# Kernel optimization log

Measured on AMD Instinct MI355X. Metric: run time of the kernel, lower is better.

## Reference

```python
import jax, jax.numpy as jnp
import numpy as np

EPS = 1e-6

def _rms(x, w):
    # RMSNorm over last dim with learned scale w
    var = jnp.mean(x * x, axis=-1, keepdims=True)
    return x * jax.lax.rsqrt(var + EPS) * w

def _split_heads(x, h):
    b, l, hd = x.shape
    return x.reshape(b, l, h, hd // h).transpose(0, 2, 1, 3)  # b h l d

def setup_inputs() -> dict:
    key = jax.random.key(0)
    ks = jax.random.split(key, 12)
    D = 2048          # hidden_size == ip_hidden_states_dim
    H = 16            # n_heads
    Dh = 128          # head_dim
    T = 1280          # timesteps_emb_dim
    B, L, Lip = 2, 2048, 512
    s = 0.02
    return {
        "ip_hidden_states": jax.random.normal(ks[0], (B, Lip, D), jnp.float32),
        "img_query": jax.random.normal(ks[1], (B, L, D), jnp.float32),
        "img_key": jax.random.normal(ks[2], (B, L, D), jnp.float32),
        "img_value": jax.random.normal(ks[3], (B, L, D), jnp.float32),
        "t_emb": jax.random.normal(ks[4], (B, T), jnp.float32),
        "W_ada": jax.random.normal(ks[5], (2 * D, T), jnp.float32) * s,
        "b_ada": jax.random.normal(ks[6], (2 * D,), jnp.float32) * s,
        "W_k_ip": jax.random.normal(ks[7], (D, D), jnp.float32) * s,
        "W_v_ip": jax.random.normal(ks[8], (D, D), jnp.float32) * s,
        "w_q": jnp.ones((Dh,), jnp.float32),
        "w_k": jnp.ones((Dh,), jnp.float32),
        "w_ipk": jnp.ones((Dh,), jnp.float32),
        "n_heads": H,
    }

def reference(ip_hidden_states, img_query, img_key, img_value, t_emb,
              W_ada, b_ada, W_k_ip, W_v_ip, w_q, w_k, w_ipk, n_heads):
    D = img_query.shape[-1]
    # AdaLayerNorm (mode='normal'): silu -> linear -> shift/scale, LN(no affine)
    emb = jax.nn.silu(t_emb) @ W_ada.T + b_ada          # [B, 2D]
    shift, scale = emb[:, :D], emb[:, D:]
    x = ip_hidden_states
    mu = jnp.mean(x, axis=-1, keepdims=True)
    var = jnp.mean((x - mu) ** 2, axis=-1, keepdims=True)
    xn = (x - mu) * jax.lax.rsqrt(var + 1e-6)
    ip_n = xn * (1.0 + scale[:, None, :]) + shift[:, None, :]
    # K/V projections for IP tokens
    ip_key = ip_n @ W_k_ip.T
    ip_value = ip_n @ W_v_ip.T
    # split heads
    q = _split_heads(img_query, n_heads)   # b h L d
    k = _split_heads(img_key, n_heads)
    v = _split_heads(img_value, n_heads)
    kip = _split_heads(ip_key, n_heads)    # b h Lip d
    vip = _split_heads(ip_value, n_heads)
    # RMSNorms
    q = _rms(q, w_q)
    k = _rms(k, w_k)
    kip = _rms(kip, w_ipk)
    # concat image + IP along sequence
    kcat = jnp.concatenate([k, kip], axis=2)
    vcat = jnp.concatenate([v, vip], axis=2)
    # SDPA
    d = q.shape[-1]
    scores = jnp.einsum('bhld,bhmd->bhlm', q, kcat) / jnp.sqrt(jnp.asarray(d, q.dtype))
    attn = jax.nn.softmax(scores, axis=-1)
    out = jnp.einsum('bhlm,bhmd->bhld', attn, vcat)
    b, h, l, dh = out.shape
    return out.transpose(0, 2, 1, 3).reshape(b, l, h * dh)
```

## Files before the change

### kernel.cpp

```cpp
#include <hip/hip_runtime.h>
#include <hip/hip_bf16.h>

typedef __attribute__((ext_vector_type(8))) __bf16 bf16x8;
typedef __attribute__((ext_vector_type(2))) __bf16 bf16x2;
typedef __attribute__((ext_vector_type(4))) float floatx4;
typedef __attribute__((ext_vector_type(2))) unsigned int uint2v;

#define DEV static __device__ __forceinline__

typedef __attribute__((address_space(1))) const unsigned int gu32;
typedef __attribute__((address_space(3))) unsigned int lu32;

DEV void dma16(const void* g, void* l) {
  __builtin_amdgcn_global_load_lds((gu32*)g, (lu32*)l, 16, 0, 0);
}

DEV unsigned short f2bf(float f) {
  unsigned int u = __float_as_uint(f);
  u += 0x7fffu + ((u >> 16) & 1u);
  return (unsigned short)(u >> 16);
}

DEV unsigned int pk_bf16(float a, float b) {
#if __has_builtin(__builtin_amdgcn_cvt_pk_bf16_f32)
  bf16x2 r = __builtin_amdgcn_cvt_pk_bf16_f32(a, b);
  union { bf16x2 v; unsigned int u; } c; c.v = r;
  return c.u;
#else
  return (unsigned int)f2bf(a) | ((unsigned int)f2bf(b) << 16);
#endif
}

DEV float wred_sum(float v) {
#pragma unroll
  for (int o = 32; o > 0; o >>= 1) v += __shfl_xor(v, o, 64);
  return v;
}

DEV floatx4 mfma32(bf16x8 a, bf16x8 b, floatx4 c) {
  return __builtin_amdgcn_mfma_f32_16x16x32_bf16(a, b, c, 0, 0, 0);
}

#if __has_builtin(__builtin_amdgcn_permlane32_swap) && __has_builtin(__builtin_amdgcn_permlane16_swap)
#define HAS_PLSWAP 1
DEV void p32sw(unsigned int& a, unsigned int& b) {
  uint2v r = __builtin_amdgcn_permlane32_swap(a, b, false, false);
  a = r[0]; b = r[1];
}
DEV void p16sw(unsigned int& a, unsigned int& b) {
  uint2v r = __builtin_amdgcn_permlane16_swap(a, b, false, false);
  a = r[0]; b = r[1];
}
#endif

__global__ void ada_kernel(const float* __restrict__ t_emb, const float* __restrict__ W_ada,
                           const float* __restrict__ b_ada, float* __restrict__ emb) {
  int w = threadIdx.x >> 6, lane = threadIdx.x & 63;
  int gid = blockIdx.x * 4 + w;
  int b = gid >> 12, n = gid & 4095;
  const float* te = t_emb + (size_t)b * 1280;
  const float* wr = W_ada + (size_t)n * 1280;
  float acc = 0.f;
#pragma unroll
  for (int i = 0; i < 20; ++i) {
    int t = lane + i * 64;
    float x = te[t];
    float s = x / (1.f + __expf(-x));
    acc += s * wr[t];
  }
  acc = wred_sum(acc);
  if (lane == 0) emb[gid] = acc + b_ada[n];
}

__global__ void ln_mod_kernel(const float* __restrict__ ip, const float* __restrict__ emb,
                              unsigned short* __restrict__ ipn) {
  int row = blockIdx.x;
  int b = row >> 9;
  const float* x = ip + (size_t)row * 2048;
  float xv[8];
  float s1 = 0.f, s2 = 0.f;
#pragma unroll
  for (int i = 0; i < 8; ++i) {
    float v = x[threadIdx.x + i * 256];
    xv[i] = v; s1 += v; s2 += v * v;
  }
  s1 = wred_sum(s1); s2 = wred_sum(s2);
  __shared__ float r1[4], r2[4];
  int w = threadIdx.x >> 6, lane = threadIdx.x & 63;
  if (lane == 0) { r1[w] = s1; r2[w] = s2; }
  __syncthreads();
  s1 = r1[0] + r1[1] + r1[2] + r1[3];
  s2 = r2[0] + r2[1] + r2[2] + r2[3];
  float mu = s1 * (1.f / 2048.f);
  float var = s2 * (1.f / 2048.f) - mu * mu;
  float rs = rsqrtf(var + 1e-6f);
  const float* sh = emb + (size_t)b * 4096;
  unsigned short* y = ipn + (size_t)row * 2048;
#pragma unroll
  for (int i = 0; i < 8; ++i) {
    int d = threadIdx.x + i * 256;
    float v = (xv[i] - mu) * rs;
    v = v * (1.f + sh[2048 + d]) + sh[d];
    y[d] = f2bf(v);
  }
}

struct us4 { unsigned short a, b, c, d; };
__global__ void cvtw_kernel(const float* __restrict__ wk, const float* __restrict__ wv,
                            unsigned short* __restrict__ wk16, unsigned short* __restrict__ wv16) {
  size_t i = ((size_t)blockIdx.x * 256 + threadIdx.x) * 4;
  float4 a = *(const float4*)(wk + i);
  float4 b = *(const float4*)(wv + i);
  us4 oa = { f2bf(a.x), f2bf(a.y), f2bf(a.z), f2bf(a.w) };
  us4 ob = { f2bf(b.x), f2bf(b.y), f2bf(b.z), f2bf(b.w) };
  *(us4*)(wk16 + i) = oa;
  *(us4*)(wv16 + i) = ob;
}

__global__ __launch_bounds__(256) void proj_gemm(const unsigned short* __restrict__ A,
    const unsigned short* __restrict__ Wk, const unsigned short* __restrict__ Wv,
    float* __restrict__ Ck, float* __restrict__ Cv) {
  const unsigned short* Bm = blockIdx.z ? Wv : Wk;
  float* C = blockIdx.z ? Cv : Ck;
  int n0 = blockIdx.x * 64, m0 = blockIdx.y * 128;
  __shared__ __align__(16) unsigned short As[128 * 72];
  __shared__ __align__(16) unsigned short Bs[64 * 72];
  int tid = threadIdx.x, w = tid >> 6, lane = tid & 63, quad = lane >> 4, l16 = lane & 15;
  floatx4 acc[2][4];
#pragma unroll
  for (int i = 0; i < 2; ++i)
#pragma unroll
    for (int j = 0; j < 4; ++j) { floatx4 z = {0.f, 0.f, 0.f, 0.f}; acc[i][j] = z; }
  for (int kk = 0; kk < 2048; kk += 64) {
#pragma unroll
    for (int it = 0; it < 4; ++it) {
      int idx = tid + it * 256;
      int row = idx >> 3, chk = idx & 7;
      *(uint4*)&As[row * 72 + chk * 8] = *(const uint4*)&A[(size_t)(m0 + row) * 2048 + kk + chk * 8];
    }
#pragma unroll
    for (int it = 0; it < 2; ++it) {
      int idx = tid + it * 256;
      int row = idx >> 3, chk = idx & 7;
      *(uint4*)&Bs[row * 72 + chk * 8] = *(const uint4*)&Bm[(size_t)(n0 + row) * 2048 + kk + chk * 8];
    }
    __syncthreads();
#pragma unroll
    for (int c = 0; c < 2; ++c) {
      bf16x8 a0 = *(const bf16x8*)&As[(w * 32 + l16) * 72 + quad * 8 + c * 32];
      bf16x8 a1 = *(const bf16x8*)&As[(w * 32 + 16 + l16) * 72 + quad * 8 + c * 32];
#pragma unroll
      for (int nt = 0; nt < 4; ++nt) {
        bf16x8 bb = *(const bf16x8*)&Bs[(nt * 16 + l16) * 72 + quad * 8 + c * 32];
        acc[0][nt] = mfma32(a0, bb, acc[0][nt]);
        acc[1][nt] = mfma32(a1, bb, acc[1][nt]);
      }
    }
    __syncthreads();
  }
#pragma unroll
  for (int rt = 0; rt < 2; ++rt)
#pragma unroll
    for (int nt = 0; nt < 4; ++nt)
#pragma unroll
      for (int r = 0; r < 4; ++r)
        C[(size_t)(m0 + w * 32 + rt * 16 + quad * 4 + r) * 2048 + n0 + nt * 16 + l16] = acc[rt][nt][r];
}

__global__ __launch_bounds__(256) void kv_build(const float* __restrict__ img_key, const float* __restrict__ img_value,
                         const float* __restrict__ ipk, const float* __restrict__ ipv,
                         const float* __restrict__ w_k, const float* __restrict__ w_ipk,
                         unsigned short* __restrict__ Kc, unsigned short* __restrict__ VtT) {
  int bh = blockIdx.x;
  int mt = blockIdx.y;
  int b = bh >> 4, hh = bh & 15;
  int m0 = mt * 64;
  __shared__ __align__(16) unsigned short Vs[64 * 132];
  int tid = threadIdx.x;
  int mrow = tid >> 2, dq = tid & 3;
  int m = m0 + mrow;
  size_t base;
  const float* wsrc;
  const float *ksrc, *vsrc;
  if (m < 2048) {
    base = (size_t)(b * 2048 + m) * 2048 + hh * 128;
    ksrc = img_key + base; vsrc = img_value + base; wsrc = w_k;
  } else {
    base = (size_t)(b * 512 + (m - 2048)) * 2048 + hh * 128;
    ksrc = ipk + base; vsrc = ipv + base; wsrc = w_ipk;
  }
  float kvv[32]; float ss = 0.f;
  const float4* k4 = (const float4*)ksrc;
#pragma unroll
  for (int i = 0; i < 8; ++i) {
    float4 x = k4[dq * 8 + i];
    kvv[i * 4 + 0] = x.x; kvv[i * 4 + 1] = x.y; kvv[i * 4 + 2] = x.z; kvv[i * 4 + 3] = x.w;
    ss += x.x * x.x + x.y * x.y + x.z * x.z + x.w * x.w;
  }
  ss += __shfl_xor(ss, 1, 64);
  ss += __shfl_xor(ss, 2, 64);
  float rs = rsqrtf(ss * (1.f / 128.f) + 1e-6f);
  unsigned short kb[32];
#pragma unroll
  for (int j = 0; j < 32; ++j) kb[j] = f2bf(kvv[j] * rs * wsrc[dq * 32 + j]);
  uint4* kdst = (uint4*)&Kc[((size_t)bh * 2560 + m) * 128];
#pragma unroll
  for (int i = 0; i < 4; ++i) kdst[(dq * 4 + i) ^ (m & 7)] = ((const uint4*)kb)[i];
  const float4* v4 = (const float4*)vsrc;
#pragma unroll
  for (int i = 0; i < 8; ++i) {
    float4 x = v4[dq * 8 + i];
    us4 p = { f2bf(x.x), f2bf(x.y), f2bf(x.z), f2bf(x.w) };
    *(us4*)&Vs[mrow * 132 + dq * 32 + i * 4] = p;
  }
  __syncthreads();
  int d = tid >> 1, half = tid & 1;
  unsigned short ob[32];
#pragma unroll
  for (int j = 0; j < 32; ++j) ob[j] = Vs[(half * 32 + j) * 132 + d];
  uint4* vdst = (uint4*)&VtT[((size_t)(bh * 40 + mt)) * 8192 + d * 64];
#pragma unroll
  for (int i = 0; i < 4; ++i) vdst[(half * 4 + i) ^ (d & 7)] = ((const uint4*)ob)[i];
}

__global__ __launch_bounds__(256, 2) void attn_kernel(const float* __restrict__ Qf,
    const float* __restrict__ w_q,
    const unsigned short* __restrict__ Kc, const unsigned short* __restrict__ VtT,
    float* __restrict__ out) {
  const float SCL = 0.12751744f;
  const float FM = 17.0f;
  int n = blockIdx.x;
  int xcd = n & 7, jj = n >> 3;
  int bh = xcd * 4 + (jj >> 4);
  int qt2 = jj & 15;
  int b = bh >> 4, hh = bh & 15;
  int tid = threadIdx.x, w = tid >> 6, lane = tid & 63, quad = lane >> 4, l16 = lane & 15;
  int xr = l16 & 7;

  __shared__ __align__(16) unsigned char smem[65536];

  int q0 = qt2 * 128;

  bf16x8 aq[2][4];
#pragma unroll
  for (int qtl = 0; qtl < 2; ++qtl) {
    int qrow = q0 + w * 32 + qtl * 16 + l16;
    const float* src = Qf + ((size_t)(b * 2048 + qrow)) * 2048 + hh * 128;
    float xs[32]; float ss = 0.f;
#pragma unroll
    for (int c = 0; c < 4; ++c) {
      float4 a = *(const float4*)&src[quad * 8 + c * 32];
      float4 b2 = *(const float4*)&src[quad * 8 + c * 32 + 4];
      xs[c * 8 + 0] = a.x;  xs[c * 8 + 1] = a.y;  xs[c * 8 + 2] = a.z;  xs[c * 8 + 3] = a.w;
      xs[c * 8 + 4] = b2.x; xs[c * 8 + 5] = b2.y; xs[c * 8 + 6] = b2.z; xs[c * 8 + 7] = b2.w;
      ss += a.x * a.x + a.y * a.y + a.z * a.z + a.w * a.w
          + b2.x * b2.x + b2.y * b2.y + b2.z * b2.z + b2.w * b2.w;
    }
    ss += __shfl_xor(ss, 16, 64);
    ss += __shfl_xor(ss, 32, 64);
    float rs = rsqrtf(ss * (1.f / 128.f) + 1e-6f);
#pragma unroll
    for (int c = 0; c < 4; ++c) {
      float4 wa = *(const float4*)&w_q[quad * 8 + c * 32];
      float4 wb = *(const float4*)&w_q[quad * 8 + c * 32 + 4];
      union { unsigned int u[4]; bf16x8 v; } pk;
      pk.u[0] = pk_bf16(xs[c * 8 + 0] * rs * wa.x, xs[c * 8 + 1] * rs * wa.y);
      pk.u[1] = pk_bf16(xs[c * 8 + 2] * rs * wa.z, xs[c * 8 + 3] * rs * wa.w);
      pk.u[2] = pk_bf16(xs[c * 8 + 4] * rs * wb.x, xs[c * 8 + 5] * rs * wb.y);
      pk.u[3] = pk_bf16(xs[c * 8 + 6] * rs * wb.z, xs[c * 8 + 7] * rs * wb.w);
      aq[qtl][c] = pk.v;
    }
  }

  const unsigned short* Kb = Kc + (size_t)bh * 2560 * 128;
  const unsigned short* Vb = VtT + (size_t)bh * 40 * 8192;

  floatx4 acc[2][8];
#pragma unroll
  for (int i = 0; i < 2; ++i)
#pragma unroll
    for (int j = 0; j < 8; ++j) { floatx4 z = {0.f, 0.f, 0.f, 0.f}; acc[i][j] = z; }
  float rsum[2] = {0.f, 0.f};

  int seg = w * 4;
  auto stage = [&](int buf, int t) {
    const unsigned short* Ksrc = Kb + (size_t)t * 8192;
    const unsigned short* Vsrc = Vb + (size_t)t * 8192;
    unsigned short* Kt = (unsigned short*)(smem + buf * 32768);
    unsigned short* Vd = (unsigned short*)(smem + buf * 32768 + 16384);
#pragma unroll
    for (int j = 0; j < 4; ++j) {
      int off = (seg + j) * 512 + lane * 8;
      dma16(Ksrc + off, Kt + (seg + j) * 512);
      dma16(Vsrc + off, Vd + (seg + j) * 512);
    }
  };

  stage(0, 0);
  __syncthreads();

  for (int t = 0; t < 40; ++t) {
    int cur = t & 1;
    if (t < 39) stage(cur ^ 1, t + 1);
    const unsigned short* Kt = (const unsigned short*)(smem + cur * 32768);
    const unsigned short* Vs = (const unsigned short*)(smem + cur * 32768 + 16384);

    floatx4 sacc[4][2];
#pragma unroll
    for (int ms = 0; ms < 4; ++ms)
#pragma unroll
      for (int j = 0; j < 2; ++j) { floatx4 z = {0.f, 0.f, 0.f, 0.f}; sacc[ms][j] = z; }
#pragma unroll
    for (int ms = 0; ms < 4; ++ms) {
      int krow = (ms * 16 + l16) * 128;
#pragma unroll
      for (int c = 0; c < 4; ++c) {
        bf16x8 bk = *(const bf16x8*)&Kt[krow + ((quad + c * 4) ^ xr) * 8];
        sacc[ms][0] = mfma32(bk, aq[0][c], sacc[ms][0]);
        sacc[ms][1] = mfma32(bk, aq[1][c], sacc[ms][1]);
      }
    }

    union { unsigned int u[4]; bf16x8 v; } pf[2][2];
#pragma unroll
    for (int mc = 0; mc < 2; ++mc) {
#pragma unroll
      for (int qtl = 0; qtl < 2; ++qtl) {
        float pA[4], pB[4];
#pragma unroll
        for (int r = 0; r < 4; ++r) {
          pA[r] = __builtin_amdgcn_exp2f(fmaf(sacc[mc * 2][qtl][r], SCL, -FM));
          pB[r] = __builtin_amdgcn_exp2f(fmaf(sacc[mc * 2 + 1][qtl][r], SCL, -FM));
        }
        rsum[qtl] += (pA[0] + pA[1]) + (pA[2] + pA[3])
                   + (pB[0] + pB[1]) + (pB[2] + pB[3]);
        unsigned int R0 = pk_bf16(pA[0], pA[1]);
        unsigned int R1 = pk_bf16(pA[2], pA[3]);
        unsigned int R2 = pk_bf16(pB[0], pB[1]);
        unsigned int R3 = pk_bf16(pB[2], pB[3]);
#ifdef HAS_PLSWAP
        p32sw(R0, R2);
        p32sw(R1, R3);
        p16sw(R0, R2);
        p16sw(R1, R3);
        pf[mc][qtl].u[0] = R0; pf[mc][qtl].u[1] = R1;
        pf[mc][qtl].u[2] = R2; pf[mc][qtl].u[3] = R3;
#else
        int base = ((quad & 1) * 2) * 16 + l16;
        int base2 = base + 16;
        unsigned int a0 = __shfl((int)R0, base, 64),  b0 = __shfl((int)R2, base, 64);
        unsigned int a1 = __shfl((int)R1, base, 64),  b1 = __shfl((int)R3, base, 64);
        unsigned int a2 = __shfl((int)R0, base2, 64), b2 = __shfl((int)R2, base2, 64);
        unsigned int a3 = __shfl((int)R1, base2, 64), b3 = __shfl((int)R3, base2, 64);
        bool hi = (quad >> 1) != 0;
        pf[mc][qtl].u[0] = hi ? b0 : a0;
        pf[mc][qtl].u[1] = hi ? b1 : a1;
        pf[mc][qtl].u[2] = hi ? b2 : a2;
        pf[mc][qtl].u[3] = hi ? b3 : a3;
#endif
      }
    }

#pragma unroll
    for (int dt = 0; dt < 8; ++dt) {
      int vrow = (dt * 16 + l16) * 64;
#pragma unroll
      for (int mc = 0; mc < 2; ++mc) {
        bf16x8 va = *(const bf16x8*)&Vs[vrow + ((mc * 4 + quad) ^ xr) * 8];
        acc[0][dt] = mfma32(va, pf[mc][0].v, acc[0][dt]);
        acc[1][dt] = mfma32(va, pf[mc][1].v, acc[1][dt]);
      }
    }
    __syncthreads();
  }

  rsum[0] += __shfl_xor(rsum[0], 16, 64); rsum[0] += __shfl_xor(rsum[0], 32, 64);
  rsum[1] += __shfl_xor(rsum[1], 16, 64); rsum[1] += __shfl_xor(rsum[1], 32, 64);
#pragma unroll
  for (int qtl = 0; qtl < 2; ++qtl) {
    float inv = 1.f / rsum[qtl];
    int qrow = q0 + w * 32 + qtl * 16 + l16;
    float* orow = out + ((size_t)(b * 2048 + qrow)) * 2048 + hh * 128;
#pragma unroll
    for (int dt = 0; dt < 8; ++dt) {
      floatx4 r = acc[qtl][dt] * inv;
      *(floatx4*)&orow[dt * 16 + quad * 4] = r;
    }
  }
}

extern "C" void kernel_launch(void* const* d_in, const int* in_sizes, int n_in,
                              void* d_out, int out_size, void* d_ws, size_t ws_size,
                              hipStream_t stream) {
  const float* ip    = (const float*)d_in[0];
  const float* q     = (const float*)d_in[1];
  const float* k     = (const float*)d_in[2];
  const float* v     = (const float*)d_in[3];
  const float* temb  = (const float*)d_in[4];
  const float* wada  = (const float*)d_in[5];
  const float* bada  = (const float*)d_in[6];
  const float* wkip  = (const float*)d_in[7];
  const float* wvip  = (const float*)d_in[8];
  const float* w_q   = (const float*)d_in[9];
  const float* w_k   = (const float*)d_in[10];
  const float* w_ipk = (const float*)d_in[11];
  float* out = (float*)d_out;
  char* ws = (char*)d_ws;

  float* emb           = (float*)(ws + 0);
  unsigned short* ipn  = (unsigned short*)(ws + 32768);
  unsigned short* wk16 = (unsigned short*)(ws + 4227072);
  unsigned short* wv16 = (unsigned short*)(ws + 12615680);
  unsigned short* Kcat = (unsigned short*)(ws + 16777216);
  unsigned short* VtT  = (unsigned short*)(ws + 37748736);
  float* ipk           = (float*)(ws + 58720256);
  float* ipv           = (float*)(ws + 67108864);

  ada_kernel<<<dim3(2048), dim3(256), 0, stream>>>(temb, wada, bada, emb);
  ln_mod_kernel<<<dim3(1024), dim3(256), 0, stream>>>(ip, emb, ipn);
  cvtw_kernel<<<dim3(4096), dim3(256), 0, stream>>>(wkip, wvip, wk16, wv16);
  proj_gemm<<<dim3(32, 8, 2), dim3(256), 0, stream>>>(ipn, wk16, wv16, ipk, ipv);
  kv_build<<<dim3(32, 40), dim3(256), 0, stream>>>(k, v, ipk, ipv, w_k, w_ipk, Kcat, VtT);
  attn_kernel<<<dim3(512), dim3(256), 0, stream>>>(q, w_q, Kcat, VtT, out);
}
```

Measured before the change: 381.4 us.

## Pre-swizzle V into MFMA fragment order and load it directly from global

kv_build now writes V tiles in the exact per-lane MFMA operand order, so attention loads V fragments straight from global memory with coalesced 16-byte reads instead of staging them through LDS. This halves the attention kernel's shared memory, and the launch-bounds occupancy hint goes from 2 to 4 blocks per CU. The QK score computation is also split per key chunk to cut live registers. The risk is that global V loads now sit on the critical path without prefetch and rely on L2 hits, and the higher occupancy target could force register spills.

```diff
diff --git a/kernel.cpp b/kernel.cpp
--- a/kernel.cpp
+++ b/kernel.cpp
@@ -170,7 +170,7 @@
 __global__ __launch_bounds__(256) void kv_build(const float* __restrict__ img_key, const float* __restrict__ img_value,
                          const float* __restrict__ ipk, const float* __restrict__ ipv,
                          const float* __restrict__ w_k, const float* __restrict__ w_ipk,
-                         unsigned short* __restrict__ Kc, unsigned short* __restrict__ VtT) {
+                         unsigned short* __restrict__ Kc, unsigned short* __restrict__ Vrec) {
   int bh = blockIdx.x;
   int mt = blockIdx.y;
   int b = bh >> 4, hh = bh & 15;
@@ -214,18 +214,23 @@
     *(us4*)&Vs[mrow * 132 + dq * 32 + i * 4] = p;
   }
   __syncthreads();
-  int d = tid >> 1, half = tid & 1;
-  unsigned short ob[32];
-#pragma unroll
-  for (int j = 0; j < 32; ++j) ob[j] = Vs[(half * 32 + j) * 132 + d];
-  uint4* vdst = (uint4*)&VtT[((size_t)(bh * 40 + mt)) * 8192 + d * 64];
-#pragma unroll
-  for (int i = 0; i < 4; ++i) vdst[(half * 4 + i) ^ (d & 7)] = ((const uint4*)ob)[i];
-}
-
-__global__ __launch_bounds__(256, 2) void attn_kernel(const float* __restrict__ Qf,
+  int lslot = tid & 63;
+  unsigned short* tb = Vrec + ((size_t)(bh * 40 + mt)) * 8192;
+#pragma unroll
+  for (int i = 0; i < 4; ++i) {
+    int r = (tid >> 6) + 4 * i;
+    int dcol = (r >> 1) * 16 + (lslot & 15);
+    int mrow2 = (r & 1) * 32 + (lslot >> 4) * 8;
+    unsigned short ob[8];
+#pragma unroll
+    for (int j = 0; j < 8; ++j) ob[j] = Vs[(mrow2 + j) * 132 + dcol];
+    *(uint4*)&tb[r * 512 + lslot * 8] = *(const uint4*)ob;
+  }
+}
+
+__global__ __launch_bounds__(256, 4) void attn_kernel(const float* __restrict__ Qf,
     const float* __restrict__ w_q,
-    const unsigned short* __restrict__ Kc, const unsigned short* __restrict__ VtT,
+    const unsigned short* __restrict__ Kc, const unsigned short* __restrict__ Vrec,
     float* __restrict__ out) {
   const float SCL = 0.12751744f;
   const float FM = 17.0f;
@@ -237,7 +242,7 @@
   int tid = threadIdx.x, w = tid >> 6, lane = tid & 63, quad = lane >> 4, l16 = lane & 15;
   int xr = l16 & 7;
 
-  __shared__ __align__(16) unsigned char smem[65536];
+  __shared__ __align__(16) unsigned char smem[32768];
 
   int q0 = qt2 * 128;
 
@@ -273,7 +278,7 @@
   }
 
   const unsigned short* Kb = Kc + (size_t)bh * 2560 * 128;
-  const unsigned short* Vb = VtT + (size_t)bh * 40 * 8192;
+  const unsigned short* Vb = Vrec + (size_t)bh * 40 * 8192;
 
   floatx4 acc[2][8];
 #pragma unroll
@@ -285,14 +290,11 @@
   int seg = w * 4;
   auto stage = [&](int buf, int t) {
     const unsigned short* Ksrc = Kb + (size_t)t * 8192;
-    const unsigned short* Vsrc = Vb + (size_t)t * 8192;
-    unsigned short* Kt = (unsigned short*)(smem + buf * 32768);
-    unsigned short* Vd = (unsigned short*)(smem + buf * 32768 + 16384);
+    unsigned short* Kt = (unsigned short*)(smem + buf * 16384);
 #pragma unroll
     for (int j = 0; j < 4; ++j) {
       int off = (seg + j) * 512 + lane * 8;
       dma16(Ksrc + off, Kt + (seg + j) * 512);
-      dma16(Vsrc + off, Vd + (seg + j) * 512);
     }
   };
 
@@ -302,35 +304,34 @@
   for (int t = 0; t < 40; ++t) {
     int cur = t & 1;
     if (t < 39) stage(cur ^ 1, t + 1);
-    const unsigned short* Kt = (const unsigned short*)(smem + cur * 32768);
-    const unsigned short* Vs = (const unsigned short*)(smem + cur * 32768 + 16384);
-
-    floatx4 sacc[4][2];
-#pragma unroll
-    for (int ms = 0; ms < 4; ++ms)
-#pragma unroll
-      for (int j = 0; j < 2; ++j) { floatx4 z = {0.f, 0.f, 0.f, 0.f}; sacc[ms][j] = z; }
-#pragma unroll
-    for (int ms = 0; ms < 4; ++ms) {
-      int krow = (ms * 16 + l16) * 128;
-#pragma unroll
-      for (int c = 0; c < 4; ++c) {
-        bf16x8 bk = *(const bf16x8*)&Kt[krow + ((quad + c * 4) ^ xr) * 8];
-        sacc[ms][0] = mfma32(bk, aq[0][c], sacc[ms][0]);
-        sacc[ms][1] = mfma32(bk, aq[1][c], sacc[ms][1]);
+    const unsigned short* Kt = (const unsigned short*)(smem + cur * 16384);
+    const unsigned short* Vr = Vb + (size_t)t * 8192;
+
+    union { unsigned int u[4]; bf16x8 v; } pf[2][2];
+#pragma unroll
+    for (int mc = 0; mc < 2; ++mc) {
+      floatx4 sacc[2][2];
+#pragma unroll
+      for (int i = 0; i < 2; ++i)
+#pragma unroll
+        for (int j = 0; j < 2; ++j) { floatx4 z = {0.f, 0.f, 0.f, 0.f}; sacc[i][j] = z; }
+#pragma unroll
+      for (int ms2 = 0; ms2 < 2; ++ms2) {
+        int krow = ((mc * 2 + ms2) * 16 + l16) * 128;
+#pragma unroll
+        for (int c = 0; c < 4; ++c) {
+          bf16x8 bk = *(const bf16x8*)&Kt[krow + ((quad + c * 4) ^ xr) * 8];
+          sacc[ms2][0] = mfma32(bk, aq[0][c], sacc[ms2][0]);
+          sacc[ms2][1] = mfma32(bk, aq[1][c], sacc[ms2][1]);
+        }
       }
-    }
-
-    union { unsigned int u[4]; bf16x8 v; } pf[2][2];
-#pragma unroll
-    for (int mc = 0; mc < 2; ++mc) {
 #pragma unroll
       for (int qtl = 0; qtl < 2; ++qtl) {
         float pA[4], pB[4];
 #pragma unroll
         for (int r = 0; r < 4; ++r) {
-          pA[r] = __builtin_amdgcn_exp2f(fmaf(sacc[mc * 2][qtl][r], SCL, -FM));
-          pB[r] = __builtin_amdgcn_exp2f(fmaf(sacc[mc * 2 + 1][qtl][r], SCL, -FM));
+          pA[r] = __builtin_amdgcn_exp2f(fmaf(sacc[0][qtl][r], SCL, -FM));
+          pB[r] = __builtin_amdgcn_exp2f(fmaf(sacc[1][qtl][r], SCL, -FM));
         }
         rsum[qtl] += (pA[0] + pA[1]) + (pA[2] + pA[3])
                    + (pB[0] + pB[1]) + (pB[2] + pB[3]);
@@ -363,13 +364,12 @@
 
 #pragma unroll
     for (int dt = 0; dt < 8; ++dt) {
-      int vrow = (dt * 16 + l16) * 64;
-#pragma unroll
-      for (int mc = 0; mc < 2; ++mc) {
-        bf16x8 va = *(const bf16x8*)&Vs[vrow + ((mc * 4 + quad) ^ xr) * 8];
-        acc[0][dt] = mfma32(va, pf[mc][0].v, acc[0][dt]);
-        acc[1][dt] = mfma32(va, pf[mc][1].v, acc[1][dt]);
-      }
+      bf16x8 va0 = *(const bf16x8*)&Vr[(dt * 2 + 0) * 512 + lane * 8];
+      bf16x8 va1 = *(const bf16x8*)&Vr[(dt * 2 + 1) * 512 + lane * 8];
+      acc[0][dt] = mfma32(va0, pf[0][0].v, acc[0][dt]);
+      acc[1][dt] = mfma32(va0, pf[0][1].v, acc[1][dt]);
+      acc[0][dt] = mfma32(va1, pf[1][0].v, acc[0][dt]);
+      acc[1][dt] = mfma32(va1, pf[1][1].v, acc[1][dt]);
     }
     __syncthreads();
   }
@@ -412,7 +412,7 @@
   unsigned short* wk16 = (unsigned short*)(ws + 4227072);
   unsigned short* wv16 = (unsigned short*)(ws + 12615680);
   unsigned short* Kcat = (unsigned short*)(ws + 16777216);
-  unsigned short* VtT  = (unsigned short*)(ws + 37748736);
+  unsigned short* Vrec = (unsigned short*)(ws + 37748736);
   float* ipk           = (float*)(ws + 58720256);
   float* ipv           = (float*)(ws + 67108864);
 
@@ -420,6 +420,6 @@
   ln_mod_kernel<<<dim3(1024), dim3(256), 0, stream>>>(ip, emb, ipn);
   cvtw_kernel<<<dim3(4096), dim3(256), 0, stream>>>(wkip, wvip, wk16, wv16);
   proj_gemm<<<dim3(32, 8, 2), dim3(256), 0, stream>>>(ipn, wk16, wv16, ipk, ipv);
-  kv_build<<<dim3(32, 40), dim3(256), 0, stream>>>(k, v, ipk, ipv, w_k, w_ipk, Kcat, VtT);
-  attn_kernel<<<dim3(512), dim3(256), 0, stream>>>(q, w_q, Kcat, VtT, out);
-}
+  kv_build<<<dim3(32, 40), dim3(256), 0, stream>>>(k, v, ipk, ipv, w_k, w_ipk, Kcat, Vrec);
+  attn_kernel<<<dim3(512), dim3(256), 0, stream>>>(q, w_q, Kcat, Vrec, out);
+}
```

After: 557.2 us. +46.1%, slower.

## Double-buffer projection GEMM with direct-to-LDS loads and XOR-swizzled operands

Applied to the files above, without the earlier changes.

The projection GEMM now stages A and B tiles into LDS with global_load_lds DMA, double-buffered so the next K tile loads while MFMAs run on the current one. The padded LDS rows are dropped in favour of an XOR swizzle of 16-byte chunks, and the swizzle is applied when producers write to global memory: LayerNorm output and weight conversion store their rows pre-permuted so the DMA copy lands in a bank-conflict-free layout. The two producer kernels are also vectorised to 8 elements per thread. This couples three kernels to one swizzled layout and removes the per-iteration sync before the next load, which depends on DMA completion ordering being correct.

```diff
diff --git a/kernel.cpp b/kernel.cpp
--- a/kernel.cpp
+++ b/kernel.cpp
@@ -76,17 +76,21 @@
                               unsigned short* __restrict__ ipn) {
   int row = blockIdx.x;
   int b = row >> 9;
+  int tid = threadIdx.x;
   const float* x = ip + (size_t)row * 2048;
   float xv[8];
   float s1 = 0.f, s2 = 0.f;
-#pragma unroll
-  for (int i = 0; i < 8; ++i) {
-    float v = x[threadIdx.x + i * 256];
-    xv[i] = v; s1 += v; s2 += v * v;
+  {
+    float4 x0 = *(const float4*)&x[tid * 8];
+    float4 x1 = *(const float4*)&x[tid * 8 + 4];
+    xv[0] = x0.x; xv[1] = x0.y; xv[2] = x0.z; xv[3] = x0.w;
+    xv[4] = x1.x; xv[5] = x1.y; xv[6] = x1.z; xv[7] = x1.w;
+#pragma unroll
+    for (int i = 0; i < 8; ++i) { s1 += xv[i]; s2 += xv[i] * xv[i]; }
   }
   s1 = wred_sum(s1); s2 = wred_sum(s2);
   __shared__ float r1[4], r2[4];
-  int w = threadIdx.x >> 6, lane = threadIdx.x & 63;
+  int w = tid >> 6, lane = tid & 63;
   if (lane == 0) { r1[w] = s1; r2[w] = s2; }
   __syncthreads();
   s1 = r1[0] + r1[1] + r1[2] + r1[3];
@@ -96,25 +100,32 @@
   float rs = rsqrtf(var + 1e-6f);
   const float* sh = emb + (size_t)b * 4096;
   unsigned short* y = ipn + (size_t)row * 2048;
+  unsigned short ob[8];
 #pragma unroll
   for (int i = 0; i < 8; ++i) {
-    int d = threadIdx.x + i * 256;
+    int d = tid * 8 + i;
     float v = (xv[i] - mu) * rs;
     v = v * (1.f + sh[2048 + d]) + sh[d];
-    y[d] = f2bf(v);
-  }
-}
-
-struct us4 { unsigned short a, b, c, d; };
+    ob[i] = f2bf(v);
+  }
+  int dst = (tid & ~7) | ((tid & 7) ^ (row & 7));
+  *(uint4*)&y[dst * 8] = *(const uint4*)ob;
+}
+
 __global__ void cvtw_kernel(const float* __restrict__ wk, const float* __restrict__ wv,
                             unsigned short* __restrict__ wk16, unsigned short* __restrict__ wv16) {
-  size_t i = ((size_t)blockIdx.x * 256 + threadIdx.x) * 4;
-  float4 a = *(const float4*)(wk + i);
-  float4 b = *(const float4*)(wv + i);
-  us4 oa = { f2bf(a.x), f2bf(a.y), f2bf(a.z), f2bf(a.w) };
-  us4 ob = { f2bf(b.x), f2bf(b.y), f2bf(b.z), f2bf(b.w) };
-  *(us4*)(wk16 + i) = oa;
-  *(us4*)(wv16 + i) = ob;
+  int row = blockIdx.x, tid = threadIdx.x;
+  size_t gi = (size_t)row * 2048 + tid * 8;
+  int dst = (tid & ~7) | ((tid & 7) ^ (row & 7));
+  size_t o = (size_t)row * 2048 + (size_t)dst * 8;
+  float4 a0 = *(const float4*)(wk + gi), a1 = *(const float4*)(wk + gi + 4);
+  float4 b0 = *(const float4*)(wv + gi), b1 = *(const float4*)(wv + gi + 4);
+  unsigned short oa[8] = { f2bf(a0.x), f2bf(a0.y), f2bf(a0.z), f2bf(a0.w),
+                           f2bf(a1.x), f2bf(a1.y), f2bf(a1.z), f2bf(a1.w) };
+  unsigned short ob[8] = { f2bf(b0.x), f2bf(b0.y), f2bf(b0.z), f2bf(b0.w),
+                           f2bf(b1.x), f2bf(b1.y), f2bf(b1.z), f2bf(b1.w) };
+  *(uint4*)(wk16 + o) = *(const uint4*)oa;
+  *(uint4*)(wv16 + o) = *(const uint4*)ob;
 }
 
 __global__ __launch_bounds__(256) void proj_gemm(const unsigned short* __restrict__ A,
@@ -123,35 +134,49 @@
   const unsigned short* Bm = blockIdx.z ? Wv : Wk;
   float* C = blockIdx.z ? Cv : Ck;
   int n0 = blockIdx.x * 64, m0 = blockIdx.y * 128;
-  __shared__ __align__(16) unsigned short As[128 * 72];
-  __shared__ __align__(16) unsigned short Bs[64 * 72];
+  __shared__ __align__(16) unsigned char smem[49152];
   int tid = threadIdx.x, w = tid >> 6, lane = tid & 63, quad = lane >> 4, l16 = lane & 15;
+  int xr = l16 & 7;
   floatx4 acc[2][4];
 #pragma unroll
   for (int i = 0; i < 2; ++i)
 #pragma unroll
     for (int j = 0; j < 4; ++j) { floatx4 z = {0.f, 0.f, 0.f, 0.f}; acc[i][j] = z; }
-  for (int kk = 0; kk < 2048; kk += 64) {
-#pragma unroll
-    for (int it = 0; it < 4; ++it) {
-      int idx = tid + it * 256;
-      int row = idx >> 3, chk = idx & 7;
-      *(uint4*)&As[row * 72 + chk * 8] = *(const uint4*)&A[(size_t)(m0 + row) * 2048 + kk + chk * 8];
-    }
-#pragma unroll
-    for (int it = 0; it < 2; ++it) {
-      int idx = tid + it * 256;
-      int row = idx >> 3, chk = idx & 7;
-      *(uint4*)&Bs[row * 72 + chk * 8] = *(const uint4*)&Bm[(size_t)(n0 + row) * 2048 + kk + chk * 8];
-    }
-    __syncthreads();
-#pragma unroll
-    for (int c = 0; c < 2; ++c) {
-      bf16x8 a0 = *(const bf16x8*)&As[(w * 32 + l16) * 72 + quad * 8 + c * 32];
-      bf16x8 a1 = *(const bf16x8*)&As[(w * 32 + 16 + l16) * 72 + quad * 8 + c * 32];
+
+  const char* Abase = (const char*)A + (size_t)m0 * 4096;
+  const char* Bbase = (const char*)Bm + (size_t)n0 * 4096;
+  auto stage = [&](int buf, int kk) {
+    char* As = (char*)(smem + buf * 24576);
+    char* Bs = (char*)(smem + buf * 24576 + 16384);
+#pragma unroll
+    for (int j = 0; j < 4; ++j) {
+      int idx = (w * 4 + j) * 64 + lane;
+      dma16(Abase + (size_t)(idx >> 3) * 4096 + kk * 2 + (idx & 7) * 16,
+            As + (w * 4 + j) * 1024);
+    }
+#pragma unroll
+    for (int j = 0; j < 2; ++j) {
+      int idx = (w * 2 + j) * 64 + lane;
+      dma16(Bbase + (size_t)(idx >> 3) * 4096 + kk * 2 + (idx & 7) * 16,
+            Bs + (w * 2 + j) * 1024);
+    }
+  };
+
+  stage(0, 0);
+  __syncthreads();
+  for (int t = 0; t < 32; ++t) {
+    int cur = t & 1;
+    if (t < 31) stage(cur ^ 1, (t + 1) * 64);
+    const unsigned short* As = (const unsigned short*)(smem + cur * 24576);
+    const unsigned short* Bs = (const unsigned short*)(smem + cur * 24576 + 16384);
+#pragma unroll
+    for (int cc = 0; cc < 2; ++cc) {
+      int pc = ((quad + 4 * cc) ^ xr) * 8;
+      bf16x8 a0 = *(const bf16x8*)&As[(w * 32 + l16) * 64 + pc];
+      bf16x8 a1 = *(const bf16x8*)&As[(w * 32 + 16 + l16) * 64 + pc];
 #pragma unroll
       for (int nt = 0; nt < 4; ++nt) {
-        bf16x8 bb = *(const bf16x8*)&Bs[(nt * 16 + l16) * 72 + quad * 8 + c * 32];
+        bf16x8 bb = *(const bf16x8*)&Bs[(nt * 16 + l16) * 64 + pc];
         acc[0][nt] = mfma32(a0, bb, acc[0][nt]);
         acc[1][nt] = mfma32(a1, bb, acc[1][nt]);
       }
@@ -167,6 +192,7 @@
         C[(size_t)(m0 + w * 32 + rt * 16 + quad * 4 + r) * 2048 + n0 + nt * 16 + l16] = acc[rt][nt][r];
 }
 
+struct us4 { unsigned short a, b, c, d; };
 __global__ __launch_bounds__(256) void kv_build(const float* __restrict__ img_key, const float* __restrict__ img_value,
                          const float* __restrict__ ipk, const float* __restrict__ ipv,
                          const float* __restrict__ w_k, const float* __restrict__ w_ipk,
@@ -418,7 +444,7 @@
 
   ada_kernel<<<dim3(2048), dim3(256), 0, stream>>>(temb, wada, bada, emb);
   ln_mod_kernel<<<dim3(1024), dim3(256), 0, stream>>>(ip, emb, ipn);
-  cvtw_kernel<<<dim3(4096), dim3(256), 0, stream>>>(wkip, wvip, wk16, wv16);
+  cvtw_kernel<<<dim3(2048), dim3(256), 0, stream>>>(wkip, wvip, wk16, wv16);
   proj_gemm<<<dim3(32, 8, 2), dim3(256), 0, stream>>>(ipn, wk16, wv16, ipk, ipv);
   kv_build<<<dim3(32, 40), dim3(256), 0, stream>>>(k, v, ipk, ipv, w_k, w_ipk, Kcat, VtT);
   attn_kernel<<<dim3(512), dim3(256), 0, stream>>>(q, w_q, Kcat, VtT, out);
```

Result: faster. 330.6 us (-13.3%).
